# Performance work log

Hardware: AMD Instinct MI355X
Metric: run time of the kernel (lower is better)

Reference implementation:

```python
import jax, jax.numpy as jnp
import numpy as np


def _lstm_layer(x, h0, c0, W_ih, W_hh, b_ih, b_hh):
    # x: [B,T,D], h0/c0: [B,H], W_ih: [4H,D], W_hh: [4H,H]
    # Precompute input contribution for all timesteps (one big GEMM).
    xg = jnp.einsum('btd,gd->btg', x, W_ih) + (b_ih + b_hh)  # [B,T,4H]

    def step(carry, xg_t):
        h, c = carry
        g = xg_t + h @ W_hh.T  # [B,4H]
        i, f, gg, o = jnp.split(g, 4, axis=-1)  # torch gate order: i,f,g,o
        i = jax.nn.sigmoid(i)
        f = jax.nn.sigmoid(f)
        gg = jnp.tanh(gg)
        o = jax.nn.sigmoid(o)
        c = f * c + i * gg
        h = o * jnp.tanh(c)
        return (h, c), h

    (hT, cT), hs = jax.lax.scan(step, (h0, c0), jnp.swapaxes(xg, 0, 1))
    return jnp.swapaxes(hs, 0, 1), hT, cT  # [B,T,H], [B,H], [B,H]


def setup_inputs() -> dict:
    key = jax.random.key(0)
    ks = jax.random.split(key, 20)
    B, T, D, H, O = 32, 2048, 64, 256, 32
    s = 0.05
    return {
        'inputs': jax.random.normal(ks[0], (B, T, D), jnp.float32),
        'h0': jax.random.normal(ks[1], (2, B, H), jnp.float32) * s,
        'c0': jax.random.normal(ks[2], (2, B, H), jnp.float32) * s,
        'W_ih0': jax.random.normal(ks[3], (4 * H, D), jnp.float32) * s,
        'W_hh0': jax.random.normal(ks[4], (4 * H, H), jnp.float32) * s,
        'b_ih0': jax.random.normal(ks[5], (4 * H,), jnp.float32) * s,
        'b_hh0': jax.random.normal(ks[6], (4 * H,), jnp.float32) * s,
        'W_ih1': jax.random.normal(ks[7], (4 * H, H), jnp.float32) * s,
        'W_hh1': jax.random.normal(ks[8], (4 * H, H), jnp.float32) * s,
        'b_ih1': jax.random.normal(ks[9], (4 * H,), jnp.float32) * s,
        'b_hh1': jax.random.normal(ks[10], (4 * H,), jnp.float32) * s,
        'W_d0': jax.random.normal(ks[11], (H, H), jnp.float32) * s,
        'b_d0': jax.random.normal(ks[12], (H,), jnp.float32) * s,
        'W_d1': jax.random.normal(ks[13], (H, H), jnp.float32) * s,
        'b_d1': jax.random.normal(ks[14], (H,), jnp.float32) * s,
        'W_out': jax.random.normal(ks[15], (O, H), jnp.float32) * s,
        'b_out': jax.random.normal(ks[16], (O,), jnp.float32) * s,
    }


def reference(inputs, h0, c0, W_ih0, W_hh0, b_ih0, b_hh0,
              W_ih1, W_hh1, b_ih1, b_hh1,
              W_d0, b_d0, W_d1, b_d1, W_out, b_out):
    # Stacked 2-layer LSTM (batch_first) matching torch nn.LSTM.
    y0, h_0, c_0 = _lstm_layer(inputs, h0[0], c0[0], W_ih0, W_hh0, b_ih0, b_hh0)
    y1, h_1, c_1 = _lstm_layer(y0, h0[1], c0[1], W_ih1, W_hh1, b_ih1, b_hh1)
    h_n = jnp.stack([h_0, h_1], axis=0)
    c_n = jnp.stack([c_0, c_1], axis=0)
    # Dense head: two Linear+ReLU, then output Linear.
    d = jax.nn.relu(jnp.einsum('bth,oh->bto', y1, W_d0) + b_d0)
    d = jax.nn.relu(jnp.einsum('bth,oh->bto', d, W_d1) + b_d1)
    out = jnp.einsum('bth,oh->bto', d, W_out) + b_out
    return out, h_n, c_n
```

## Files before the change

kernel.cpp:

```cpp
#include <hip/hip_runtime.h>
#include <hip/hip_bf16.h>
#include <cstddef>
#include <cstdint>

#define BB 32
#define TT 2048
#define DD 64
#define HH 256
#define OO 32
#define NBLK 8

#define OUT_ELEMS (BB*TT*OO)
#define HN_OFF OUT_ELEMS
#define CN_OFF (HN_OFF + 2*BB*HH)

#define O_XBF   ((size_t)0)
#define O_H0    ((size_t)8388608)
#define O_XH1   ((size_t)41959424)
#define O_WP0   ((size_t)109101056)
#define O_WP1   ((size_t)109756416)
#define O_B0    ((size_t)110804992)
#define O_B1    ((size_t)110809088)
#define O_WD0T  ((size_t)110813184)
#define O_WD1T  ((size_t)111075328)
#define O_WOUT  ((size_t)111337472)
#define O_D0    ((size_t)111370240)
#define O_D1    (O_D0 + 256)

typedef short short8 __attribute__((ext_vector_type(8)));
typedef float f32x4 __attribute__((ext_vector_type(4)));

__device__ __forceinline__ float sigm_(float x){ return 1.0f/(1.0f+__expf(-x)); }
__device__ __forceinline__ float tanhf_(float x){
    float xc = fminf(fmaxf(x, -15.0f), 15.0f);
    float e = __expf(2.0f*xc);
    return (e-1.0f)/(e+1.0f);
}
__device__ __forceinline__ unsigned short f2bf(float f){
    __hip_bfloat16 h = __float2bfloat16(f);
    return *reinterpret_cast<unsigned short*>(&h);
}
__device__ __forceinline__ unsigned int pack2(float a, float b){
    return (unsigned int)f2bf(a) | ((unsigned int)f2bf(b) << 16);
}
__device__ __forceinline__ short8 ld8(const unsigned short* p){
    return *reinterpret_cast<const short8*>(p);
}

__device__ __forceinline__ void pollLine(const int* flags, int tgt, int lane){
    int it = 0;
    while (true) {
        int v = tgt;
        if (lane < NBLK)
            v = __hip_atomic_load(flags + lane, __ATOMIC_RELAXED, __HIP_MEMORY_SCOPE_AGENT);
        if (__all(v >= tgt)) break;
        __builtin_amdgcn_s_sleep(1);
        if (++it > (1<<16)) break;
    }
    asm volatile("" ::: "memory");
}

__device__ __forceinline__ void pollTwo(const int* f0, int t0,
                                        const int* f1, int t1, int lane){
    const int* p = (lane < 8) ? (f0 + lane) : (f1 + (lane - 8));
    const int tgt = (lane < 8) ? t0 : t1;
    int it = 0;
    while (true) {
        int v = tgt;
        if (lane < 16)
            v = __hip_atomic_load(p, __ATOMIC_RELAXED, __HIP_MEMORY_SCOPE_AGENT);
        if (__all(v >= tgt)) break;
        __builtin_amdgcn_s_sleep(1);
        if (++it > (1<<16)) break;
    }
    asm volatile("" ::: "memory");
}

__global__ void prep_kernel(const float* __restrict__ x, const float* __restrict__ h0,
    const float* __restrict__ Wih0, const float* __restrict__ Whh0,
    const float* __restrict__ bih0, const float* __restrict__ bhh0,
    const float* __restrict__ Wih1, const float* __restrict__ Whh1,
    const float* __restrict__ bih1, const float* __restrict__ bhh1,
    const float* __restrict__ Wd0, const float* __restrict__ Wd1,
    const float* __restrict__ Wout, char* __restrict__ ws)
{
    int i = blockIdx.x*256 + threadIdx.x;
    if (i < 4194304) {
        int t = i >> 11, rem = i & 2047, b = rem >> 6, d = rem & 63;
        ((unsigned short*)(ws+O_XBF))[i] = f2bf(x[(size_t)b*131072 + t*64 + d]);
        return;
    }
    i -= 4194304;
    if (i < 327680) {
        int R = i / 320, k = i - R*320;
        int lrow = R & 15, s = (R>>4)&1, hr = (R>>5)&3, jj = R>>7;
        int gate = 2*s + (lrow>>3);
        int h = 32*jj + 8*hr + (lrow&7);
        int src = 256*gate + h;
        float v = (k < 64) ? Wih0[src*64 + k] : Whh0[src*256 + (k-64)];
        ((unsigned short*)(ws+O_WP0))[i] = f2bf(v);
        return;
    }
    i -= 327680;
    if (i < 524288) {
        int R = i >> 9, k = i & 511;
        int lrow = R & 15, s = (R>>4)&1, hr = (R>>5)&3, jj = R>>7;
        int gate = 2*s + (lrow>>3);
        int h = 32*jj + 8*hr + (lrow&7);
        int src = 256*gate + h;
        float v = (k < 256) ? Wih1[src*256 + k] : Whh1[src*256 + (k-256)];
        ((unsigned short*)(ws+O_WP1))[i] = f2bf(v);
        return;
    }
    i -= 524288;
    if (i < 1024) { ((float*)(ws+O_B0))[i] = bih0[i] + bhh0[i]; return; }
    i -= 1024;
    if (i < 1024) { ((float*)(ws+O_B1))[i] = bih1[i] + bhh1[i]; return; }
    i -= 1024;
    if (i < 8192) { ((unsigned short*)(ws+O_H0))[i] = f2bf(h0[i]); return; }
    i -= 8192;
    if (i < 8192) {
        int b = i >> 8, h = i & 255;
        ((unsigned short*)(ws+O_XH1))[b*512 + 256 + h] = f2bf(h0[8192 + i]);
        return;
    }
    i -= 8192;
    if (i < 65536) { int o = i & 255, h = i >> 8; ((float*)(ws+O_WD0T))[i] = Wd0[o*256 + h]; return; }
    i -= 65536;
    if (i < 65536) { int o = i & 255, h = i >> 8; ((float*)(ws+O_WD1T))[i] = Wd1[o*256 + h]; return; }
    i -= 65536;
    if (i < 8192) { int o = i & 31, h = i >> 5; ((float*)(ws+O_WOUT))[i] = Wout[o*256 + h]; return; }
    i -= 8192;
    if (i < 4096) { ((int*)(ws+O_D0))[i] = 0; return; }
}

template<int L>
__device__ void lstm_body(int j, char* ws, const float* __restrict__ c0_in,
                          float* __restrict__ out)
{
    constexpr int KK  = L ? 512 : 320;
    constexpr int NKT = KK / 32;

    const int tid  = threadIdx.x;
    const int wv   = tid >> 6;
    const int lane = tid & 63;
    const int bh   = wv >> 2;
    const int hr   = wv & 3;
    const int lrow = lane & 15;
    const int q    = lane >> 4;
    const int koff = q * 8;
    const int qe   = q & 1;
    const int fb   = bh*16 + lrow;
    const int hbase= 32*j + 8*hr + 4*qe;
    const bool lo  = (lane < 32);

    const unsigned short* Wp = (const unsigned short*)(ws + (L ? O_WP1 : O_WP0));
    const float* bias = (const float*)(ws + (L ? O_B1 : O_B0));

    const int wavebase = (j*4 + hr) * 32;
    short8 a0[NKT], a1[NKT];
#pragma unroll
    for (int kk = 0; kk < NKT; ++kk) {
        a0[kk] = ld8(Wp + (size_t)(wavebase +      lrow)*KK + kk*32 + koff);
        a1[kk] = ld8(Wp + (size_t)(wavebase + 16 + lrow)*KK + kk*32 + koff);
    }

    float bi[4], bf_[4], bg[4], bo[4], c[4], hv[4];
#pragma unroll
    for (int r = 0; r < 4; ++r) {
        int hg = hbase + r;
        bi[r] = bias[hg];       bf_[r] = bias[256+hg];
        bg[r] = bias[512+hg];   bo[r]  = bias[768+hg];
        c[r]  = c0_in[(size_t)L*8192 + fb*256 + hg];
        hv[r] = 0.f;
    }

    int* flags0 = (int*)(ws + O_D0);
    int* flags1 = (int*)(ws + O_D1);
    int* myflag = (L ? flags1 : flags0) + j;

    const unsigned short* xb = (const unsigned short*)(ws + O_XBF) + fb*64  + koff;
    const unsigned short* hb = (const unsigned short*)(ws + O_H0)  + fb*256 + koff;
    const unsigned short* xh = (const unsigned short*)(ws + O_XH1) + fb*512 + koff;

    unsigned long long* stA;
    unsigned long long* stB = nullptr;
    if (L == 0) {
        stA = (unsigned long long*)((unsigned short*)(ws + O_H0)  + (size_t)8192 + fb*256 + hbase);
        stB = (unsigned long long*)((unsigned short*)(ws + O_XH1) + (size_t)fb*512 + hbase);
    } else {
        stA = (unsigned long long*)((unsigned short*)(ws + O_XH1) + (size_t)16384 + fb*512 + 256 + hbase);
    }

    for (int t = 0; t < TT; ++t) {
        f32x4 A0 = {0.f,0.f,0.f,0.f}, A1 = {0.f,0.f,0.f,0.f};

        if (L == 0) {
            short8 bx0 = ld8(xb), bx1 = ld8(xb + 32);
            A0 = __builtin_amdgcn_mfma_f32_16x16x32_bf16(a0[0], bx0, A0, 0,0,0);
            A1 = __builtin_amdgcn_mfma_f32_16x16x32_bf16(a1[0], bx0, A1, 0,0,0);
            A0 = __builtin_amdgcn_mfma_f32_16x16x32_bf16(a0[1], bx1, A0, 0,0,0);
            A1 = __builtin_amdgcn_mfma_f32_16x16x32_bf16(a1[1], bx1, A1, 0,0,0);

            if (wv == 0) pollLine(flags0, t, lane);
            __syncthreads();

            short8 b[8];
#pragma unroll
            for (int kk = 0; kk < 8; ++kk) b[kk] = ld8(hb + 32*kk);
#pragma unroll
            for (int kk = 0; kk < 8; ++kk) {
                A0 = __builtin_amdgcn_mfma_f32_16x16x32_bf16(a0[2+kk], b[kk], A0, 0,0,0);
                A1 = __builtin_amdgcn_mfma_f32_16x16x32_bf16(a1[2+kk], b[kk], A1, 0,0,0);
            }
        } else {
            if (wv == 0) pollTwo(flags0, t+1, flags1, t, lane);
            __syncthreads();

            short8 b[8];
#pragma unroll
            for (int kk = 0; kk < 8; ++kk) b[kk] = ld8(xh + 32*kk);
#pragma unroll
            for (int kk = 0; kk < 8; ++kk) {
                A0 = __builtin_amdgcn_mfma_f32_16x16x32_bf16(a0[kk], b[kk], A0, 0,0,0);
                A1 = __builtin_amdgcn_mfma_f32_16x16x32_bf16(a1[kk], b[kk], A1, 0,0,0);
            }
#pragma unroll
            for (int kk = 0; kk < 8; ++kk) b[kk] = ld8(xh + 256 + 32*kk);
#pragma unroll
            for (int kk = 0; kk < 8; ++kk) {
                A0 = __builtin_amdgcn_mfma_f32_16x16x32_bf16(a0[8+kk], b[kk], A0, 0,0,0);
                A1 = __builtin_amdgcn_mfma_f32_16x16x32_bf16(a1[8+kk], b[kk], A1, 0,0,0);
            }
        }

#pragma unroll
        for (int r = 0; r < 4; ++r) {
            float x0 = A0[r], y0 = __shfl_xor(x0, 32, 64);
            float x1 = A1[r], y1 = __shfl_xor(x1, 32, 64);
            float gi = (lo ? x0 : y0) + bi[r];
            float gf = (lo ? y0 : x0) + bf_[r];
            float gg = (lo ? x1 : y1) + bg[r];
            float go = (lo ? y1 : x1) + bo[r];
            float iv = sigm_(gi), fv = sigm_(gf), gv = tanhf_(gg), ov = sigm_(go);
            c[r]  = fv*c[r] + iv*gv;
            hv[r] = ov * tanhf_(c[r]);
        }

        unsigned long long w =
            (unsigned long long)pack2(hv[0], hv[1]) |
            ((unsigned long long)pack2(hv[2], hv[3]) << 32);

        if (L == 0) {
            if (lo) __hip_atomic_store(stA, w, __ATOMIC_RELAXED, __HIP_MEMORY_SCOPE_AGENT);
            else    __hip_atomic_store(stB, w, __ATOMIC_RELAXED, __HIP_MEMORY_SCOPE_AGENT);
        } else {
            if (lo) __hip_atomic_store(stA, w, __ATOMIC_RELAXED, __HIP_MEMORY_SCOPE_AGENT);
        }

        __syncthreads();
        if (tid == 0)
            __hip_atomic_store(myflag, t+1, __ATOMIC_RELAXED, __HIP_MEMORY_SCOPE_AGENT);

        xb += 2048; hb += 8192; xh += 16384;
        stA += (L ? 4096 : 2048);
        if (L == 0) stB += 4096;
    }

    if (lo) {
#pragma unroll
        for (int r = 0; r < 4; ++r) {
            out[HN_OFF + (size_t)L*8192 + fb*256 + hbase + r] = hv[r];
            out[CN_OFF + (size_t)L*8192 + fb*256 + hbase + r] = c[r];
        }
    }
}

__global__ __launch_bounds__(512, 2) void lstm_fused(char* ws,
                                                     const float* __restrict__ c0_in,
                                                     float* __restrict__ out)
{
    if (blockIdx.x < NBLK) lstm_body<0>(blockIdx.x, ws, c0_in, out);
    else                   lstm_body<1>(blockIdx.x - NBLK, ws, c0_in, out);
}

__global__ __launch_bounds__(256) void head_kernel(const char* __restrict__ ws,
    const float* __restrict__ bd0, const float* __restrict__ bd1,
    const float* __restrict__ bout, float* __restrict__ out)
{
    const __hip_bfloat16* xh1 = (const __hip_bfloat16*)(ws + O_XH1);
    const float* Wd0T  = (const float*)(ws + O_WD0T);
    const float* Wd1T  = (const float*)(ws + O_WD1T);
    const float* WoutT = (const float*)(ws + O_WOUT);

    __shared__ float buf0[16][256];
    __shared__ float buf1[16][256];
    const int row0 = blockIdx.x * 16;
    const int tid = threadIdx.x;

#pragma unroll
    for (int i = 0; i < 16; ++i) {
        int r = row0 + i;
        int b = r >> 11, t = r & 2047;
        buf0[i][tid] = __bfloat162float(xh1[(size_t)(t+1)*16384 + b*512 + 256 + tid]);
    }
    __syncthreads();

    {
        float acc[16];
        float bv = bd0[tid];
#pragma unroll
        for (int r = 0; r < 16; ++r) acc[r] = bv;
        for (int h = 0; h < 256; ++h) {
            float w = Wd0T[h*256 + tid];
#pragma unroll
            for (int r = 0; r < 16; ++r) acc[r] += w * buf0[r][h];
        }
        __syncthreads();
#pragma unroll
        for (int r = 0; r < 16; ++r) buf1[r][tid] = fmaxf(acc[r], 0.0f);
    }
    __syncthreads();

    {
        float acc[16];
        float bv = bd1[tid];
#pragma unroll
        for (int r = 0; r < 16; ++r) acc[r] = bv;
        for (int h = 0; h < 256; ++h) {
            float w = Wd1T[h*256 + tid];
#pragma unroll
            for (int r = 0; r < 16; ++r) acc[r] += w * buf1[r][h];
        }
        __syncthreads();
#pragma unroll
        for (int r = 0; r < 16; ++r) buf0[r][tid] = fmaxf(acc[r], 0.0f);
    }
    __syncthreads();

    {
        const int o = tid & 31;
        const int rr = tid >> 5;
        float a0 = bout[o], a1 = bout[o];
        for (int h = 0; h < 256; ++h) {
            float w = WoutT[h*32 + o];
            a0 += w * buf0[rr*2 + 0][h];
            a1 += w * buf0[rr*2 + 1][h];
        }
        out[(size_t)(row0 + rr*2 + 0)*32 + o] = a0;
        out[(size_t)(row0 + rr*2 + 1)*32 + o] = a1;
    }
}

extern "C" void kernel_launch(void* const* d_in, const int* in_sizes, int n_in,
                              void* d_out, int out_size, void* d_ws, size_t ws_size,
                              hipStream_t stream) {
    const float* x    = (const float*)d_in[0];
    const float* h0   = (const float*)d_in[1];
    const float* c0   = (const float*)d_in[2];
    const float* Wih0 = (const float*)d_in[3];
    const float* Whh0 = (const float*)d_in[4];
    const float* bih0 = (const float*)d_in[5];
    const float* bhh0 = (const float*)d_in[6];
    const float* Wih1 = (const float*)d_in[7];
    const float* Whh1 = (const float*)d_in[8];
    const float* bih1 = (const float*)d_in[9];
    const float* bhh1 = (const float*)d_in[10];
    const float* Wd0  = (const float*)d_in[11];
    const float* bd0  = (const float*)d_in[12];
    const float* Wd1  = (const float*)d_in[13];
    const float* bd1  = (const float*)d_in[14];
    const float* Wout = (const float*)d_in[15];
    const float* bout = (const float*)d_in[16];

    char* ws = (char*)d_ws;
    float* out = (float*)d_out;

    prep_kernel<<<20344, 256, 0, stream>>>(x, h0, Wih0, Whh0, bih0, bhh0,
                                           Wih1, Whh1, bih1, bhh1,
                                           Wd0, Wd1, Wout, ws);
    lstm_fused<<<2*NBLK, 512, 0, stream>>>(ws, c0, out);
    head_kernel<<<4096, 256, 0, stream>>>(ws, bd0, bd1, bout, out);
}
```

Baseline: 12.10 ms.

## Replace block-wide barriers with per-batch-half wave counters and flags

Drops the per-timestep __syncthreads barriers. Each wave now polls the cross-block flags for its own batch half, and a shared-memory atomic counter per half and timestep lets the fourth-arriving wave publish the block's flag. The two batch halves of the recurrence can then advance independently and wave-level latency is not serialized by block barriers. In exchange every wave polls global memory, and correctness depends on the vmcnt wait and the relaxed atomics giving enough visibility ordering.

```diff
diff --git a/kernel.cpp b/kernel.cpp
--- a/kernel.cpp
+++ b/kernel.cpp
@@ -24,8 +24,7 @@
 #define O_WD0T  ((size_t)110813184)
 #define O_WD1T  ((size_t)111075328)
 #define O_WOUT  ((size_t)111337472)
-#define O_D0    ((size_t)111370240)
-#define O_D1    (O_D0 + 256)
+#define O_FLG   ((size_t)111370240)
 
 typedef short short8 __attribute__((ext_vector_type(8)));
 typedef float f32x4 __attribute__((ext_vector_type(4)));
@@ -47,7 +46,7 @@
     return *reinterpret_cast<const short8*>(p);
 }
 
-__device__ __forceinline__ void pollLine(const int* flags, int tgt, int lane){
+__device__ __forceinline__ void pollHalf(const int* flags, int tgt, int lane){
     int it = 0;
     while (true) {
         int v = tgt;
@@ -60,8 +59,8 @@
     asm volatile("" ::: "memory");
 }
 
-__device__ __forceinline__ void pollTwo(const int* f0, int t0,
-                                        const int* f1, int t1, int lane){
+__device__ __forceinline__ void pollHalf2(const int* f0, int t0,
+                                          const int* f1, int t1, int lane){
     const int* p = (lane < 8) ? (f0 + lane) : (f1 + (lane - 8));
     const int tgt = (lane < 8) ? t0 : t1;
     int it = 0;
@@ -131,12 +130,12 @@
     i -= 65536;
     if (i < 8192) { int o = i & 31, h = i >> 5; ((float*)(ws+O_WOUT))[i] = Wout[o*256 + h]; return; }
     i -= 8192;
-    if (i < 4096) { ((int*)(ws+O_D0))[i] = 0; return; }
+    if (i < 4096) { ((int*)(ws+O_FLG))[i] = 0; return; }
 }
 
 template<int L>
 __device__ void lstm_body(int j, char* ws, const float* __restrict__ c0_in,
-                          float* __restrict__ out)
+                          float* __restrict__ out, int* __restrict__ ctr)
 {
     constexpr int KK  = L ? 512 : 320;
     constexpr int NKT = KK / 32;
@@ -175,9 +174,10 @@
         hv[r] = 0.f;
     }
 
-    int* flags0 = (int*)(ws + O_D0);
-    int* flags1 = (int*)(ws + O_D1);
-    int* myflag = (L ? flags1 : flags0) + j;
+    int* F0h = (int*)(ws + O_FLG) + bh*16;
+    int* F1h = (int*)(ws + O_FLG) + 64 + bh*16;
+    int* myflag = (L ? F1h : F0h) + j;
+    int* myctr  = ctr + bh;
 
     const unsigned short* xb = (const unsigned short*)(ws + O_XBF) + fb*64  + koff;
     const unsigned short* hb = (const unsigned short*)(ws + O_H0)  + fb*256 + koff;
@@ -202,8 +202,7 @@
             A0 = __builtin_amdgcn_mfma_f32_16x16x32_bf16(a0[1], bx1, A0, 0,0,0);
             A1 = __builtin_amdgcn_mfma_f32_16x16x32_bf16(a1[1], bx1, A1, 0,0,0);
 
-            if (wv == 0) pollLine(flags0, t, lane);
-            __syncthreads();
+            pollHalf(F0h, t, lane);
 
             short8 b[8];
 #pragma unroll
@@ -214,8 +213,7 @@
                 A1 = __builtin_amdgcn_mfma_f32_16x16x32_bf16(a1[2+kk], b[kk], A1, 0,0,0);
             }
         } else {
-            if (wv == 0) pollTwo(flags0, t+1, flags1, t, lane);
-            __syncthreads();
+            pollHalf2(F0h, t+1, F1h, t, lane);
 
             short8 b[8];
 #pragma unroll
@@ -258,9 +256,13 @@
             if (lo) __hip_atomic_store(stA, w, __ATOMIC_RELAXED, __HIP_MEMORY_SCOPE_AGENT);
         }
 
-        __syncthreads();
-        if (tid == 0)
-            __hip_atomic_store(myflag, t+1, __ATOMIC_RELAXED, __HIP_MEMORY_SCOPE_AGENT);
+        asm volatile("s_waitcnt vmcnt(0)" ::: "memory");
+        if (lane == 0) {
+            int old = atomicAdd(myctr + t*2, 1);
+            if (old == 3)
+                __hip_atomic_store(myflag, t+1,
+                                   __ATOMIC_RELAXED, __HIP_MEMORY_SCOPE_AGENT);
+        }
 
         xb += 2048; hb += 8192; xh += 16384;
         stA += (L ? 4096 : 2048);
@@ -280,8 +282,12 @@
                                                      const float* __restrict__ c0_in,
                                                      float* __restrict__ out)
 {
-    if (blockIdx.x < NBLK) lstm_body<0>(blockIdx.x, ws, c0_in, out);
-    else                   lstm_body<1>(blockIdx.x - NBLK, ws, c0_in, out);
+    __shared__ int ctr[2*TT];
+    for (int i = threadIdx.x; i < 2*TT; i += 512) ctr[i] = 0;
+    __syncthreads();
+
+    if (blockIdx.x < NBLK) lstm_body<0>(blockIdx.x, ws, c0_in, out, ctr);
+    else                   lstm_body<1>(blockIdx.x - NBLK, ws, c0_in, out, ctr);
 }
 
 __global__ __launch_bounds__(256) void head_kernel(const char* __restrict__ ws,
```

Result: slower. 13.13 ms, median of 2 (+8.5%).

## Replace block-level barriers with per-wave tag flags for cross-block LSTM sync

Applied to the files above, without the earlier changes.

Each wave now publishes its own progress tag after waiting for its stores to complete, and every wave polls the 32 producer-wave tags it depends on directly. This removes the two __syncthreads per timestep and the single-wave poll followed by a block barrier. The serial recurrence's per-step latency should drop, at the cost of more polling traffic from all waves and a subtler memory-ordering guarantee that relies on s_waitcnt rather than a barrier.

```diff
diff --git a/kernel.cpp b/kernel.cpp
--- a/kernel.cpp
+++ b/kernel.cpp
@@ -24,8 +24,7 @@
 #define O_WD0T  ((size_t)110813184)
 #define O_WD1T  ((size_t)111075328)
 #define O_WOUT  ((size_t)111337472)
-#define O_D0    ((size_t)111370240)
-#define O_D1    (O_D0 + 256)
+#define O_TAG   ((size_t)111370240)
 
 typedef short short8 __attribute__((ext_vector_type(8)));
 typedef float f32x4 __attribute__((ext_vector_type(4)));
@@ -47,12 +46,12 @@
     return *reinterpret_cast<const short8*>(p);
 }
 
-__device__ __forceinline__ void pollLine(const int* flags, int tgt, int lane){
+__device__ __forceinline__ void pollTags(const int* tags, int tgt, int lane){
     int it = 0;
     while (true) {
         int v = tgt;
-        if (lane < NBLK)
-            v = __hip_atomic_load(flags + lane, __ATOMIC_RELAXED, __HIP_MEMORY_SCOPE_AGENT);
+        if (lane < 32)
+            v = __hip_atomic_load(tags + lane, __ATOMIC_RELAXED, __HIP_MEMORY_SCOPE_AGENT);
         if (__all(v >= tgt)) break;
         __builtin_amdgcn_s_sleep(1);
         if (++it > (1<<16)) break;
@@ -60,15 +59,13 @@
     asm volatile("" ::: "memory");
 }
 
-__device__ __forceinline__ void pollTwo(const int* f0, int t0,
-                                        const int* f1, int t1, int lane){
-    const int* p = (lane < 8) ? (f0 + lane) : (f1 + (lane - 8));
-    const int tgt = (lane < 8) ? t0 : t1;
+__device__ __forceinline__ void pollTags2(const int* t0a, int tgt0,
+                                          const int* t1a, int tgt1, int lane){
+    const int* p = (lane < 32) ? (t0a + lane) : (t1a + (lane - 32));
+    const int tgt = (lane < 32) ? tgt0 : tgt1;
     int it = 0;
     while (true) {
-        int v = tgt;
-        if (lane < 16)
-            v = __hip_atomic_load(p, __ATOMIC_RELAXED, __HIP_MEMORY_SCOPE_AGENT);
+        int v = __hip_atomic_load(p, __ATOMIC_RELAXED, __HIP_MEMORY_SCOPE_AGENT);
         if (__all(v >= tgt)) break;
         __builtin_amdgcn_s_sleep(1);
         if (++it > (1<<16)) break;
@@ -131,7 +128,7 @@
     i -= 65536;
     if (i < 8192) { int o = i & 31, h = i >> 5; ((float*)(ws+O_WOUT))[i] = Wout[o*256 + h]; return; }
     i -= 8192;
-    if (i < 4096) { ((int*)(ws+O_D0))[i] = 0; return; }
+    if (i < 4096) { ((int*)(ws+O_TAG))[i] = 0; return; }
 }
 
 template<int L>
@@ -175,9 +172,9 @@
         hv[r] = 0.f;
     }
 
-    int* flags0 = (int*)(ws + O_D0);
-    int* flags1 = (int*)(ws + O_D1);
-    int* myflag = (L ? flags1 : flags0) + j;
+    int* T0h = (int*)(ws + O_TAG) + bh*32;
+    int* T1h = (int*)(ws + O_TAG + 1024) + bh*32;
+    int* mytag = (L ? T1h : T0h) + (j*4 + hr);
 
     const unsigned short* xb = (const unsigned short*)(ws + O_XBF) + fb*64  + koff;
     const unsigned short* hb = (const unsigned short*)(ws + O_H0)  + fb*256 + koff;
@@ -202,8 +199,7 @@
             A0 = __builtin_amdgcn_mfma_f32_16x16x32_bf16(a0[1], bx1, A0, 0,0,0);
             A1 = __builtin_amdgcn_mfma_f32_16x16x32_bf16(a1[1], bx1, A1, 0,0,0);
 
-            if (wv == 0) pollLine(flags0, t, lane);
-            __syncthreads();
+            pollTags(T0h, t, lane);
 
             short8 b[8];
 #pragma unroll
@@ -214,8 +210,7 @@
                 A1 = __builtin_amdgcn_mfma_f32_16x16x32_bf16(a1[2+kk], b[kk], A1, 0,0,0);
             }
         } else {
-            if (wv == 0) pollTwo(flags0, t+1, flags1, t, lane);
-            __syncthreads();
+            pollTags2(T0h, t+1, T1h, t, lane);
 
             short8 b[8];
 #pragma unroll
@@ -258,9 +253,9 @@
             if (lo) __hip_atomic_store(stA, w, __ATOMIC_RELAXED, __HIP_MEMORY_SCOPE_AGENT);
         }
 
-        __syncthreads();
-        if (tid == 0)
-            __hip_atomic_store(myflag, t+1, __ATOMIC_RELAXED, __HIP_MEMORY_SCOPE_AGENT);
+        asm volatile("s_waitcnt vmcnt(0)" ::: "memory");
+        if (lane == 0)
+            __hip_atomic_store(mytag, t+1, __ATOMIC_RELAXED, __HIP_MEMORY_SCOPE_AGENT);
 
         xb += 2048; hb += 8192; xh += 16384;
         stA += (L ? 4096 : 2048);
```

Measured after the change: 15.85 ms. 31.0% more time.
